# Kernel tuning notes

Measured on AMD Instinct MI355X. Metric: run time of the kernel, lower is better.

The kernel has to match this reference:

```python
import jax, jax.numpy as jnp
import numpy as np

N_NODES = 50000
N_EDGES = 800000
F_IN = 32
H = 128
N_REL = 4
MAX_DEG = 10
N_GRAPHS = 64
N_BLOCKS = 2


def setup_inputs() -> dict:
    key = jax.random.key(0)
    ks = jax.random.split(key, 20)
    s = 0.05
    return {
        "x": jax.random.normal(ks[0], (N_NODES, F_IN), jnp.float32),
        "edge_index": jax.random.randint(ks[1], (2, N_EDGES), 0, N_NODES, dtype=jnp.int32),
        "edge_attr": jax.random.randint(ks[2], (N_EDGES,), 0, N_REL, dtype=jnp.int32),
        "batch_idx": jnp.sort(jax.random.randint(ks[3], (N_NODES,), 0, N_GRAPHS, dtype=jnp.int32)),
        "embed_W": jax.random.normal(ks[4], (F_IN, H), jnp.float32) * s,
        "embed_b": jax.random.normal(ks[5], (H,), jnp.float32) * s,
        "rgcn_Wrel": jax.random.normal(ks[6], (N_BLOCKS, N_REL, H, H), jnp.float32) * s,
        "rgcn_Wroot": jax.random.normal(ks[7], (N_BLOCKS, H, H), jnp.float32) * s,
        "rgcn_b": jax.random.normal(ks[8], (N_BLOCKS, H), jnp.float32) * s,
        "mf_Wl": jax.random.normal(ks[9], (N_BLOCKS, MAX_DEG + 1, H, H), jnp.float32) * s,
        "mf_bl": jax.random.normal(ks[10], (N_BLOCKS, MAX_DEG + 1, H), jnp.float32) * s,
        "mf_Wr": jax.random.normal(ks[11], (N_BLOCKS, MAX_DEG + 1, H, H), jnp.float32) * s,
        "lin1_W": jax.random.normal(ks[12], (H, H), jnp.float32) * s,
        "lin1_b": jax.random.normal(ks[13], (H,), jnp.float32) * s,
        "lin2_W": jax.random.normal(ks[14], (H, 1), jnp.float32) * s,
        "lin2_b": jax.random.normal(ks[15], (1,), jnp.float32) * s,
    }


def _rgcn(x, src, dst, rel, Wrel, Wroot, b):
    # PyG RGCNConv with default aggr='mean': per-relation mean over incoming
    # edges, then per-relation weight, plus root transform and bias.
    seg = dst * N_REL + rel  # composite segment id: (node, relation)
    agg = jax.ops.segment_sum(x[src], seg, num_segments=N_NODES * N_REL)
    cnt = jax.ops.segment_sum(jnp.ones((seg.shape[0],), x.dtype), seg,
                              num_segments=N_NODES * N_REL)
    agg = (agg / jnp.maximum(cnt, 1.0)[:, None]).reshape(N_NODES, N_REL, H)
    return jnp.einsum('nrh,rho->no', agg, Wrel) + x @ Wroot + b


def _mfconv(x, src, dst, Wl, bl, Wr):
    # PyG MFConv: sum-aggregate neighbors, then per-degree-bucket linear heads
    # (degree = in-degree clamped to MAX_DEG); lin_r applied to root x (no bias).
    h = jax.ops.segment_sum(x[src], dst, num_segments=N_NODES)  # [N,H]
    deg = jax.ops.segment_sum(jnp.ones((src.shape[0],), jnp.int32), dst,
                              num_segments=N_NODES)
    deg = jnp.minimum(deg, MAX_DEG)  # [N]
    # out_all: [D+1, N, H] candidate outputs, one per degree bucket
    out_all = (jnp.einsum('nh,dho->dno', h, Wl)
               + jnp.einsum('nh,dho->dno', x, Wr)
               + bl[:, None, :])
    return jnp.take_along_axis(out_all, deg[None, :, None], axis=0)[0]


def reference(x, edge_index, edge_attr, batch_idx, embed_W, embed_b,
              rgcn_Wrel, rgcn_Wroot, rgcn_b, mf_Wl, mf_bl, mf_Wr,
              lin1_W, lin1_b, lin2_W, lin2_b):
    src, dst = edge_index[0], edge_index[1]
    h = x @ embed_W + embed_b
    for blk in range(N_BLOCKS):
        if blk > 0:  # first block uses Identity instead of ReLU
            h = jax.nn.relu(h)
        h = _rgcn(h, src, dst, edge_attr, rgcn_Wrel[blk], rgcn_Wroot[blk], rgcn_b[blk])
        h = jax.nn.relu(h)
        h = _mfconv(h, src, dst, mf_Wl[blk], mf_bl[blk], mf_Wr[blk])
    g = jax.ops.segment_sum(h, batch_idx, num_segments=N_GRAPHS)  # global_add_pool
    g = jax.nn.relu(g @ lin1_W + lin1_b)
    return g @ lin2_W + lin2_b
```

## Files before the change

### kernel.cpp

```cpp
#include <hip/hip_runtime.h>
#include <hip/hip_bf16.h>

#define NRELS 4
#define MAXDEG 10
#define NBUCK 11
#define POOL_CHUNKS 8

typedef __attribute__((ext_vector_type(8))) short s16x8;
typedef __attribute__((ext_vector_type(4))) float f32x4;
typedef __attribute__((ext_vector_type(8))) unsigned short u16x8;

__device__ inline unsigned short f2b(float f) {
  __hip_bfloat16 h = __float2bfloat16(f);
  return *reinterpret_cast<unsigned short*>(&h);
}
__device__ inline float b2f(unsigned short u) {
  union { unsigned int i; float f; } v;
  v.i = ((unsigned int)u) << 16;
  return v.f;
}
__device__ inline float blo(unsigned int v) {
  union { unsigned int i; float f; } x;
  x.i = v << 16;
  return x.f;
}
__device__ inline float bhi(unsigned int v) {
  union { unsigned int i; float f; } x;
  x.i = v & 0xffff0000u;
  return x.f;
}

typedef __attribute__((address_space(3))) unsigned int lds_uint;
typedef __attribute__((address_space(1))) const unsigned int glob_uint;
__device__ __forceinline__ void gld_lds16(const void* g, void* l) {
  __builtin_amdgcn_global_load_lds((glob_uint*)g, (lds_uint*)l, 16, 0, 0);
}

__global__ __launch_bounds__(512) void coarse_count(const int* __restrict__ dst,
                                                    int* __restrict__ bhist, int E) {
  __shared__ int lh[512];
  int t = threadIdx.x;
  lh[t] = 0;
  __syncthreads();
  int base = blockIdx.x * 4096;
  int lim = E - base;
  if (lim > 4096) lim = 4096;
  for (int i = t; i < lim; i += 512) atomicAdd(&lh[dst[base + i] >> 7], 1);
  __syncthreads();
  if (lh[t]) atomicAdd(&bhist[t], lh[t]);
}

__global__ __launch_bounds__(512) void coarse_scan(const int* __restrict__ bhist,
                                                   int* __restrict__ boff,
                                                   int* __restrict__ bcur, int NB, int E) {
  __shared__ int sd[512];
  int t = threadIdx.x;
  int v = (t < NB) ? bhist[t] : 0;
  sd[t] = v;
  __syncthreads();
  for (int o = 1; o < 512; o <<= 1) {
    int x = (t >= o) ? sd[t - o] : 0;
    __syncthreads();
    sd[t] += x;
    __syncthreads();
  }
  if (t < NB) {
    int st = sd[t] - v;
    boff[t] = st;
    bcur[t] = st;
  }
  if (t == 0) boff[NB] = E;
}

__global__ __launch_bounds__(512) void coarse_scatter(
    const int* __restrict__ src, const int* __restrict__ dst, const int* __restrict__ rel,
    int* __restrict__ bcur, uint2* __restrict__ ebuf, int E) {
  __shared__ int lhist[512];
  __shared__ int lstart[512];
  __shared__ int lcur[512];
  __shared__ int gbase[512];
  __shared__ uint2 stage[4096];
  int t = threadIdx.x;
  lhist[t] = 0;
  __syncthreads();
  int base = blockIdx.x * 4096;
  int lim = E - base;
  if (lim > 4096) lim = 4096;
  for (int i = t; i < lim; i += 512) atomicAdd(&lhist[dst[base + i] >> 7], 1);
  __syncthreads();
  int myc = lhist[t];
  lstart[t] = myc;
  __syncthreads();
  for (int o = 1; o < 512; o <<= 1) {
    int x = (t >= o) ? lstart[t - o] : 0;
    __syncthreads();
    lstart[t] += x;
    __syncthreads();
  }
  int incl = lstart[t];
  __syncthreads();
  lstart[t] = incl - myc;
  lcur[t] = 0;
  if (myc > 0) gbase[t] = atomicAdd(&bcur[t], myc);
  __syncthreads();
  for (int i = t; i < lim; i += 512) {
    int e = base + i;
    int d = dst[e];
    int b = d >> 7;
    int slot = lstart[b] + atomicAdd(&lcur[b], 1);
    stage[slot] = make_uint2((unsigned)(d * 4 + rel[e]), (unsigned)src[e]);
  }
  __syncthreads();
  for (int i = t; i < lim; i += 512) {
    uint2 val = stage[i];
    int b = (int)(val.x >> 9);
    ebuf[gbase[b] + (i - lstart[b])] = val;
  }
}

__global__ __launch_bounds__(512) void fine_count_scan(
    const uint2* __restrict__ ebuf, const int* __restrict__ boff, int* __restrict__ cnt,
    int* __restrict__ seg_start, float* __restrict__ inv, int* __restrict__ deg,
    int* __restrict__ bucket, int* __restrict__ hist, int NSEG) {
  __shared__ int lh[512];
  __shared__ int sc[512];
  __shared__ int lbh[16];
  int t = threadIdx.x;
  int b = blockIdx.x;
  lh[t] = 0;
  if (t < 16) lbh[t] = 0;
  __syncthreads();
  int s = boff[b], e = boff[b + 1];
  for (int i = s + t; i < e; i += 512) atomicAdd(&lh[ebuf[i].x & 511], 1);
  __syncthreads();
  int v = lh[t];
  sc[t] = v;
  __syncthreads();
  for (int o = 1; o < 512; o <<= 1) {
    int x = (t >= o) ? sc[t - o] : 0;
    __syncthreads();
    sc[t] += x;
    __syncthreads();
  }
  int gseg = b * 512 + t;
  if (gseg < NSEG) {
    cnt[gseg] = v;
    seg_start[gseg] = s + sc[t] - v;
    inv[gseg] = 1.0f / (float)(v > 1 ? v : 1);
    if ((t & 3) == 0) {
      int d = sc[t + 3] - sc[t] + v;
      int n = gseg >> 2;
      deg[n] = d;
      int bk = d < MAXDEG ? d : MAXDEG;
      bucket[n] = bk;
      atomicAdd(&lbh[bk], 1);
    }
  }
  __syncthreads();
  if (t < NBUCK && lbh[t]) atomicAdd(&hist[t], lbh[t]);
}

__global__ __launch_bounds__(512) void place_local(const uint2* __restrict__ ebuf,
                                                   const int* __restrict__ boff,
                                                   const int* __restrict__ seg_start,
                                                   int* __restrict__ csr, int NSEG) {
  __shared__ int lcur[512];
  int t = threadIdx.x;
  int b = blockIdx.x;
  int gseg = b * 512 + t;
  lcur[t] = (gseg < NSEG) ? seg_start[gseg] : 0;
  __syncthreads();
  int s = boff[b], e = boff[b + 1];
  for (int i = s + t; i < e; i += 512) {
    uint2 v = ebuf[i];
    int pos = atomicAdd(&lcur[v.x & 511], 1);
    csr[pos] = (int)v.y;
  }
}

__global__ void build_perm(const int* __restrict__ bucket, const int* __restrict__ hist,
                           int* __restrict__ fill, int* __restrict__ perm, int N) {
  __shared__ int soff[NBUCK];
  if (threadIdx.x == 0) {
    int acc = 0;
    for (int b = 0; b < NBUCK; b++) {
      soff[b] = acc;
      acc += ((hist[b] + 63) >> 6) << 6;
    }
  }
  __syncthreads();
  int n = blockIdx.x * 256 + threadIdx.x;
  int b = (n < N) ? bucket[n] : -1;
  int lane = threadIdx.x & 63;
  for (int bb = 0; bb < NBUCK; bb++) {
    unsigned long long m = __ballot(b == bb);
    if (m == 0ULL) continue;
    int leader = __ffsll(m) - 1;
    int base = 0;
    if (lane == leader) base = atomicAdd(&fill[bb], __popcll(m));
    base = __shfl(base, leader);
    if (b == bb) {
      int idx = __popcll(m & ((1ULL << lane) - 1ULL));
      perm[soff[bb] + base + idx] = n;
    }
  }
}

__global__ void conv_weights(const float* __restrict__ Wrel, const float* __restrict__ Wroot,
                             const float* __restrict__ Wl, const float* __restrict__ Wr,
                             const float* __restrict__ embW, unsigned short* __restrict__ Bt,
                             unsigned short* __restrict__ Btm, unsigned short* __restrict__ Bte) {
  const int R1 = 2 * 128 * 640;
  const int R2 = R1 + 2 * 11 * 128 * 256;
  const int R3 = R2 + 128 * 32;
  int t = blockIdx.x * 256 + threadIdx.x;
  if (t < R1) {
    int blk = t / 81920;
    int rem = t % 81920;
    int n = rem / 640;
    int k = rem % 640;
    float v;
    if (k < 512)
      v = Wrel[(size_t)blk * 65536 + (size_t)k * 128 + n];
    else
      v = Wroot[(size_t)blk * 16384 + (size_t)(k - 512) * 128 + n];
    Bt[t] = f2b(v);
    return;
  }
  if (t < R2) {
    int t2 = t - R1;
    int k = t2 & 255;
    int n = (t2 >> 8) & 127;
    int bb = (t2 >> 15) % 11;
    int blk = t2 / (11 * 128 * 256);
    float v;
    if (k < 128)
      v = Wl[(((size_t)blk * 11 + bb) * 128 + k) * 128 + n];
    else
      v = Wr[(((size_t)blk * 11 + bb) * 128 + (k - 128)) * 128 + n];
    Btm[t2] = f2b(v);
    return;
  }
  if (t < R3) {
    int t3 = t - R2;
    int n = t3 >> 5, k = t3 & 31;
    Bte[t3] = f2b(embW[(size_t)k * 128 + n]);
  }
}

#define ACC8(v)                                   \
  do {                                            \
    a0 += blo((v).x); a1 += bhi((v).x);           \
    a2 += blo((v).y); a3 += bhi((v).y);           \
    a4 += blo((v).z); a5 += bhi((v).z);           \
    a6 += blo((v).w); a7 += bhi((v).w);           \
  } while (0)

__global__ __launch_bounds__(256) void rgcn_gather(
    const unsigned short* __restrict__ hb, const int* __restrict__ csr,
    const int* __restrict__ seg_start, const int* __restrict__ cnt,
    const float* __restrict__ inv, const int* __restrict__ perm,
    unsigned short* __restrict__ ahat, int total) {
  int half = blockIdx.x & 1;
  int i = (blockIdx.x >> 1) * 32 + (threadIdx.x >> 3);
  if (i >= total) return;
  int n = perm[i];
  if (n < 0) return;
  int c8 = half * 64 + (threadIdx.x & 7) * 8;
#pragma unroll
  for (int r = 0; r < 4; r++) {
    int seg = n * 4 + r;
    int st = seg_start[seg], cn = cnt[seg];
    float w = inv[seg];
    float a0 = 0.f, a1 = 0.f, a2 = 0.f, a3 = 0.f, a4 = 0.f, a5 = 0.f, a6 = 0.f, a7 = 0.f;
    int ii = 0;
    for (; ii + 4 <= cn; ii += 4) {
      int p0 = csr[st + ii], p1 = csr[st + ii + 1];
      int p2 = csr[st + ii + 2], p3 = csr[st + ii + 3];
      uint4 v0 = *(const uint4*)(hb + (size_t)p0 * 128 + c8);
      uint4 v1 = *(const uint4*)(hb + (size_t)p1 * 128 + c8);
      uint4 v2 = *(const uint4*)(hb + (size_t)p2 * 128 + c8);
      uint4 v3 = *(const uint4*)(hb + (size_t)p3 * 128 + c8);
      ACC8(v0);
      ACC8(v1);
      ACC8(v2);
      ACC8(v3);
    }
    if (ii + 2 <= cn) {
      int p0 = csr[st + ii], p1 = csr[st + ii + 1];
      uint4 v0 = *(const uint4*)(hb + (size_t)p0 * 128 + c8);
      uint4 v1 = *(const uint4*)(hb + (size_t)p1 * 128 + c8);
      ACC8(v0);
      ACC8(v1);
      ii += 2;
    }
    if (ii < cn) {
      uint4 v0 = *(const uint4*)(hb + (size_t)csr[st + ii] * 128 + c8);
      ACC8(v0);
    }
    uint4 o;
    o.x = (unsigned int)f2b(a0 * w) | ((unsigned int)f2b(a1 * w) << 16);
    o.y = (unsigned int)f2b(a2 * w) | ((unsigned int)f2b(a3 * w) << 16);
    o.z = (unsigned int)f2b(a4 * w) | ((unsigned int)f2b(a5 * w) << 16);
    o.w = (unsigned int)f2b(a6 * w) | ((unsigned int)f2b(a7 * w) << 16);
    *(uint4*)(ahat + (size_t)i * 512 + r * 128 + c8) = o;
  }
}

__global__ __launch_bounds__(256) void mf_gather(
    const unsigned short* __restrict__ hb, const int* __restrict__ csr,
    const int* __restrict__ seg_start, const int* __restrict__ deg,
    const int* __restrict__ perm, unsigned short* __restrict__ amf, int total) {
  int half = blockIdx.x & 1;
  int i = (blockIdx.x >> 1) * 32 + (threadIdx.x >> 3);
  if (i >= total) return;
  int n = perm[i];
  if (n < 0) return;
  int c8 = half * 64 + (threadIdx.x & 7) * 8;
  int st = seg_start[n * 4], dg = deg[n];
  float a0 = 0.f, a1 = 0.f, a2 = 0.f, a3 = 0.f, a4 = 0.f, a5 = 0.f, a6 = 0.f, a7 = 0.f;
  int i2 = 0;
  for (; i2 + 4 <= dg; i2 += 4) {
    int p0 = csr[st + i2], p1 = csr[st + i2 + 1];
    int p2 = csr[st + i2 + 2], p3 = csr[st + i2 + 3];
    uint4 v0 = *(const uint4*)(hb + (size_t)p0 * 128 + c8);
    uint4 v1 = *(const uint4*)(hb + (size_t)p1 * 128 + c8);
    uint4 v2 = *(const uint4*)(hb + (size_t)p2 * 128 + c8);
    uint4 v3 = *(const uint4*)(hb + (size_t)p3 * 128 + c8);
    ACC8(v0);
    ACC8(v1);
    ACC8(v2);
    ACC8(v3);
  }
  if (i2 + 2 <= dg) {
    int p0 = csr[st + i2], p1 = csr[st + i2 + 1];
    uint4 v0 = *(const uint4*)(hb + (size_t)p0 * 128 + c8);
    uint4 v1 = *(const uint4*)(hb + (size_t)p1 * 128 + c8);
    ACC8(v0);
    ACC8(v1);
    i2 += 2;
  }
  if (i2 < dg) {
    uint4 v0 = *(const uint4*)(hb + (size_t)csr[st + i2] * 128 + c8);
    ACC8(v0);
  }
  uint4 o;
  o.x = (unsigned int)f2b(a0) | ((unsigned int)f2b(a1) << 16);
  o.y = (unsigned int)f2b(a2) | ((unsigned int)f2b(a3) << 16);
  o.z = (unsigned int)f2b(a4) | ((unsigned int)f2b(a5) << 16);
  o.w = (unsigned int)f2b(a6) | ((unsigned int)f2b(a7) << 16);
  *(uint4*)(amf + (size_t)i * 128 + c8) = o;
}

__global__ __launch_bounds__(256) void rgcn_mfma(const unsigned short* __restrict__ A,
                                                 const unsigned short* __restrict__ hroot,
                                                 const unsigned short* __restrict__ Bt,
                                                 const float* __restrict__ bias,
                                                 const int* __restrict__ perm,
                                                 unsigned short* __restrict__ out) {
  __shared__ unsigned char As[8192];
  __shared__ unsigned char Bs[16384];
  __shared__ int nodes[64];
  int t = threadIdx.x;
  int m0 = blockIdx.x * 64;
  if (t >= 64 && t < 128) nodes[t - 64] = perm[m0 + t - 64];
  __syncthreads();
  int lane = t & 63, wave = t >> 6;
  int row = lane & 15, quad = lane >> 4;
  int nh = wave * 32;
  f32x4 acc[2][4];
#pragma unroll
  for (int i = 0; i < 2; i++)
#pragma unroll
    for (int j = 0; j < 4; j++) acc[i][j] = (f32x4){0.f, 0.f, 0.f, 0.f};

  for (int kt = 0; kt < 10; kt++) {
    int kb2 = kt * 128;
#pragma unroll
    for (int s = 0; s < 2; s++) {
      int o = s * 4096 + t * 16;
      int r = o >> 7, c = ((o >> 4) & 7) ^ (r & 7);
      const char* gsrc;
      if (kt < 8) {
        gsrc = (const char*)A + (size_t)(m0 + r) * 1024 + kb2 + c * 16;
      } else {
        int nd = nodes[r];
        if (nd < 0) nd = 0;
        gsrc = (const char*)hroot + (size_t)nd * 256 + (kb2 - 1024) + c * 16;
      }
      gld_lds16(gsrc, As + o);
    }
#pragma unroll
    for (int s = 0; s < 4; s++) {
      int o = s * 4096 + t * 16;
      int r = o >> 7, c = ((o >> 4) & 7) ^ (r & 7);
      gld_lds16((const char*)Bt + (size_t)r * 1280 + kb2 + c * 16, Bs + o);
    }
    __syncthreads();
#pragma unroll
    for (int ks = 0; ks < 2; ks++) {
      int cch = ks * 4 + quad;
      s16x8 af[4], bf[2];
#pragma unroll
      for (int mt = 0; mt < 4; mt++) {
        int R = mt * 16 + row;
        af[mt] = *(const s16x8*)(As + R * 128 + ((cch ^ (R & 7)) << 4));
      }
#pragma unroll
      for (int nt = 0; nt < 2; nt++) {
        int R = nh + nt * 16 + row;
        bf[nt] = *(const s16x8*)(Bs + R * 128 + ((cch ^ (R & 7)) << 4));
      }
#pragma unroll
      for (int nt = 0; nt < 2; nt++)
#pragma unroll
        for (int mt = 0; mt < 4; mt++)
          acc[nt][mt] = __builtin_amdgcn_mfma_f32_16x16x32_bf16(af[mt], bf[nt], acc[nt][mt], 0, 0, 0);
    }
    __syncthreads();
  }
#pragma unroll
  for (int nt = 0; nt < 2; nt++) {
    int n = nh + nt * 16 + row;
    float bv = bias[n];
#pragma unroll
    for (int mt = 0; mt < 4; mt++) {
#pragma unroll
      for (int r4 = 0; r4 < 4; r4++) {
        int nd = nodes[mt * 16 + quad * 4 + r4];
        if (nd >= 0) out[(size_t)nd * 128 + n] = f2b(fmaxf(acc[nt][mt][r4] + bv, 0.f));
      }
    }
  }
}

__global__ __launch_bounds__(256) void mf_mfma(const unsigned short* __restrict__ A,
                                               const unsigned short* __restrict__ hroot,
                                               const unsigned short* __restrict__ Bt,
                                               const float* __restrict__ bl,
                                               const int* __restrict__ perm,
                                               const int* __restrict__ hist,
                                               unsigned short* __restrict__ out, int relu_out) {
  __shared__ unsigned char As[8192];
  __shared__ unsigned char Bs[16384];
  __shared__ int soff[NBUCK + 1];
  __shared__ int nodes[64];
  int t = threadIdx.x;
  int m0 = blockIdx.x * 64;
  if (t == 0) {
    int acc = 0;
    for (int b2 = 0; b2 < NBUCK; b2++) {
      soff[b2] = acc;
      acc += ((hist[b2] + 63) >> 6) << 6;
    }
    soff[NBUCK] = acc;
  }
  if (t >= 64 && t < 128) nodes[t - 64] = perm[m0 + t - 64];
  __syncthreads();
  if (m0 >= soff[NBUCK]) return;
  int b = 0;
  while (b < 10 && m0 >= soff[b + 1]) b++;
  const unsigned short* Bb = Bt + (size_t)b * 128 * 256;
  const float* bb = bl + b * 128;
  int lane = t & 63, wave = t >> 6;
  int row = lane & 15, quad = lane >> 4;
  int nh = wave * 32;
  f32x4 acc[2][4];
#pragma unroll
  for (int i = 0; i < 2; i++)
#pragma unroll
    for (int j = 0; j < 4; j++) acc[i][j] = (f32x4){0.f, 0.f, 0.f, 0.f};

  for (int kt = 0; kt < 4; kt++) {
    int kb2 = kt * 128;
#pragma unroll
    for (int s = 0; s < 2; s++) {
      int o = s * 4096 + t * 16;
      int r = o >> 7, c = ((o >> 4) & 7) ^ (r & 7);
      const char* gsrc;
      if (kt < 2) {
        gsrc = (const char*)A + (size_t)(m0 + r) * 256 + kb2 + c * 16;
      } else {
        int nd = nodes[r];
        if (nd < 0) nd = 0;
        gsrc = (const char*)hroot + (size_t)nd * 256 + (kb2 - 512) + c * 16;
      }
      gld_lds16(gsrc, As + o);
    }
#pragma unroll
    for (int s = 0; s < 4; s++) {
      int o = s * 4096 + t * 16;
      int r = o >> 7, c = ((o >> 4) & 7) ^ (r & 7);
      gld_lds16((const char*)Bb + (size_t)r * 512 + kb2 + c * 16, Bs + o);
    }
    __syncthreads();
#pragma unroll
    for (int ks = 0; ks < 2; ks++) {
      int cch = ks * 4 + quad;
      s16x8 af[4], bf[2];
#pragma unroll
      for (int mt = 0; mt < 4; mt++) {
        int R = mt * 16 + row;
        af[mt] = *(const s16x8*)(As + R * 128 + ((cch ^ (R & 7)) << 4));
      }
#pragma unroll
      for (int nt = 0; nt < 2; nt++) {
        int R = nh + nt * 16 + row;
        bf[nt] = *(const s16x8*)(Bs + R * 128 + ((cch ^ (R & 7)) << 4));
      }
#pragma unroll
      for (int nt = 0; nt < 2; nt++)
#pragma unroll
        for (int mt = 0; mt < 4; mt++)
          acc[nt][mt] = __builtin_amdgcn_mfma_f32_16x16x32_bf16(af[mt], bf[nt], acc[nt][mt], 0, 0, 0);
    }
    __syncthreads();
  }
#pragma unroll
  for (int nt = 0; nt < 2; nt++) {
    int n = nh + nt * 16 + row;
    float bv = bb[n];
#pragma unroll
    for (int mt = 0; mt < 4; mt++) {
#pragma unroll
      for (int r4 = 0; r4 < 4; r4++) {
        int nd = nodes[mt * 16 + quad * 4 + r4];
        if (nd >= 0) {
          float v = acc[nt][mt][r4] + bv;
          if (relu_out) v = fmaxf(v, 0.f);
          out[(size_t)nd * 128 + n] = f2b(v);
        }
      }
    }
  }
}

__global__ __launch_bounds__(256) void embed_mfma(const float* __restrict__ x,
                                                  const unsigned short* __restrict__ Bte,
                                                  const float* __restrict__ bias,
                                                  unsigned short* __restrict__ out, int N) {
  __shared__ unsigned char As[64 * 80];
  __shared__ unsigned char Bs[128 * 80];
  int t = threadIdx.x;
  int m0 = blockIdx.x * 64;
  {
    int r = t >> 2, s = t & 3;
    int gr = m0 + r;
    if (gr >= N) gr = N - 1;
    const float* xp = x + (size_t)gr * 32 + s * 8;
    float4 f0 = *(const float4*)xp;
    float4 f1 = *(const float4*)(xp + 4);
    u16x8 o;
    o[0] = f2b(f0.x); o[1] = f2b(f0.y); o[2] = f2b(f0.z); o[3] = f2b(f0.w);
    o[4] = f2b(f1.x); o[5] = f2b(f1.y); o[6] = f2b(f1.z); o[7] = f2b(f1.w);
    *(u16x8*)(As + r * 80 + s * 16) = o;
  }
  {
    int n = t >> 1, s = t & 1;
    const unsigned short* bp = Bte + (size_t)n * 32 + s * 16;
    uint4 v0 = *(const uint4*)bp;
    uint4 v1 = *(const uint4*)(bp + 8);
    *(uint4*)(Bs + n * 80 + s * 32) = v0;
    *(uint4*)(Bs + n * 80 + s * 32 + 16) = v1;
  }
  __syncthreads();
  int lane = t & 63, wave = t >> 6;
  int row = lane & 15, quad = lane >> 4;
  int nh = wave * 32;
  f32x4 acc[2][4];
#pragma unroll
  for (int i = 0; i < 2; i++)
#pragma unroll
    for (int j = 0; j < 4; j++) acc[i][j] = (f32x4){0.f, 0.f, 0.f, 0.f};
  s16x8 af[4], bf[2];
#pragma unroll
  for (int mt = 0; mt < 4; mt++) {
    int R = mt * 16 + row;
    af[mt] = *(const s16x8*)(As + R * 80 + quad * 16);
  }
#pragma unroll
  for (int nt = 0; nt < 2; nt++) {
    int R = nh + nt * 16 + row;
    bf[nt] = *(const s16x8*)(Bs + R * 80 + quad * 16);
  }
#pragma unroll
  for (int nt = 0; nt < 2; nt++)
#pragma unroll
    for (int mt = 0; mt < 4; mt++)
      acc[nt][mt] = __builtin_amdgcn_mfma_f32_16x16x32_bf16(af[mt], bf[nt], acc[nt][mt], 0, 0, 0);
#pragma unroll
  for (int nt = 0; nt < 2; nt++) {
    int n = nh + nt * 16 + row;
    float bv = bias[n];
#pragma unroll
    for (int mt = 0; mt < 4; mt++) {
#pragma unroll
      for (int r4 = 0; r4 < 4; r4++) {
        int m = m0 + mt * 16 + quad * 4 + r4;
        if (m < N) out[(size_t)m * 128 + n] = f2b(acc[nt][mt][r4] + bv);
      }
    }
  }
}

__global__ void pool2(const unsigned short* __restrict__ h, const int* __restrict__ batch,
                      float* __restrict__ g, int N, int G) {
  int gr = blockIdx.x / POOL_CHUNKS;
  int ck = blockIdx.x % POOL_CHUNKS;
  int c = threadIdx.x;
  int lo = 0, hi = N;
  while (lo < hi) {
    int m = (lo + hi) >> 1;
    if (batch[m] < gr) lo = m + 1; else hi = m;
  }
  int s = lo;
  lo = s; hi = N;
  while (lo < hi) {
    int m = (lo + hi) >> 1;
    if (batch[m] < gr + 1) lo = m + 1; else hi = m;
  }
  int e = lo;
  int len = e - s;
  int a = s + (int)(((long long)len * ck) / POOL_CHUNKS);
  int b = s + (int)(((long long)len * (ck + 1)) / POOL_CHUNKS);
  float sum = 0.f;
  for (int n = a; n < b; n++) sum += b2f(h[(size_t)n * 128 + c]);
  if (b > a) atomicAdd(&g[gr * 128 + c], sum);
}

__global__ void head_kernel(const float* __restrict__ g, const float* __restrict__ W1,
                            const float* __restrict__ b1, const float* __restrict__ W2,
                            const float* __restrict__ b2, float* __restrict__ out) {
  int bg = blockIdx.x;
  int o = threadIdx.x;
  __shared__ float gs[128];
  __shared__ float red[128];
  gs[o] = g[bg * 128 + o];
  __syncthreads();
  float acc = b1[o];
  for (int k = 0; k < 128; k++) acc += gs[k] * W1[k * 128 + o];
  acc = fmaxf(acc, 0.f);
  red[o] = acc * W2[o];
  __syncthreads();
  for (int s = 64; s > 0; s >>= 1) {
    if (o < s) red[o] += red[o + s];
    __syncthreads();
  }
  if (o == 0) out[bg] = red[0] + b2[0];
}

extern "C" void kernel_launch(void* const* d_in, const int* in_sizes, int n_in,
                              void* d_out, int out_size, void* d_ws, size_t ws_size,
                              hipStream_t stream) {
  const float* x = (const float*)d_in[0];
  const int* ei = (const int*)d_in[1];
  const int* ea = (const int*)d_in[2];
  const int* batch = (const int*)d_in[3];
  const float* embW = (const float*)d_in[4];
  const float* embB = (const float*)d_in[5];
  const float* Wrel = (const float*)d_in[6];
  const float* Wroot = (const float*)d_in[7];
  const float* rb = (const float*)d_in[8];
  const float* Wl = (const float*)d_in[9];
  const float* bl = (const float*)d_in[10];
  const float* Wr = (const float*)d_in[11];
  const float* l1W = (const float*)d_in[12];
  const float* l1b = (const float*)d_in[13];
  const float* l2W = (const float*)d_in[14];
  const float* l2b = (const float*)d_in[15];
  float* out = (float*)d_out;

  int N = in_sizes[0] / 32;
  int E = in_sizes[2];
  int G = out_size;
  int NSEG = N * 4;
  int NB = (N + 127) >> 7;

  char* p = (char*)d_ws;
  auto alloc = [&](size_t bytes) {
    char* r = p;
    p += (bytes + 255) & ~(size_t)255;
    return r;
  };
  int permCap = ((N + 63) / 64 + NBUCK) * 64;
  unsigned short* h_bf = (unsigned short*)alloc((size_t)N * 128 * 2);
  unsigned short* h2_bf = (unsigned short*)alloc((size_t)N * 128 * 2);
  unsigned short* ahat = (unsigned short*)alloc((size_t)permCap * 512 * 2);
  unsigned short* amf = (unsigned short*)alloc((size_t)permCap * 128 * 2);
  unsigned short* Btr = (unsigned short*)alloc((size_t)2 * 128 * 640 * 2);
  unsigned short* Btm = (unsigned short*)alloc((size_t)2 * 11 * 128 * 256 * 2);
  unsigned short* Bte = (unsigned short*)alloc((size_t)128 * 32 * 2);
  float* inv = (float*)alloc((size_t)NSEG * 4);
  int* cnt = (int*)alloc((size_t)NSEG * 4);
  int* seg_start = (int*)alloc((size_t)NSEG * 4);
  int* csr = (int*)alloc((size_t)E * 4);
  uint2* ebuf = (uint2*)alloc((size_t)E * 8);
  int* deg = (int*)alloc((size_t)N * 4);
  int* bucket = (int*)alloc((size_t)N * 4);
  int* perm = (int*)alloc((size_t)permCap * 4);
  int* boff = (int*)alloc(516 * 4);
  int* bcur = (int*)alloc(512 * 4);
  size_t zeroBytes = 8192 + (size_t)G * 128 * 4;
  char* zb = alloc(zeroBytes);
  int* bhist = (int*)zb;
  int* hist = (int*)(zb + 4096);
  int* fill = (int*)(zb + 4224);
  float* g = (float*)(zb + 8192);

  hipMemsetAsync(zb, 0, zeroBytes, stream);
  hipMemsetAsync(perm, 0xFF, (size_t)permCap * 4, stream);

  const int* src = ei;
  const int* dst = ei + E;

  int sblocks = (E + 4095) / 4096;
  coarse_count<<<sblocks, 512, 0, stream>>>(dst, bhist, E);
  coarse_scan<<<1, 512, 0, stream>>>(bhist, boff, bcur, NB, E);
  coarse_scatter<<<sblocks, 512, 0, stream>>>(src, dst, ea, bcur, ebuf, E);
  fine_count_scan<<<NB, 512, 0, stream>>>(ebuf, boff, cnt, seg_start, inv, deg, bucket, hist,
                                          NSEG);
  build_perm<<<(N + 255) / 256, 256, 0, stream>>>(bucket, hist, fill, perm, N);
  place_local<<<NB, 512, 0, stream>>>(ebuf, boff, seg_start, csr, NSEG);
  int convTotal = 2 * 128 * 640 + 2 * 11 * 128 * 256 + 128 * 32;
  conv_weights<<<(convTotal + 255) / 256, 256, 0, stream>>>(Wrel, Wroot, Wl, Wr, embW, Btr,
                                                            Btm, Bte);

  embed_mfma<<<(N + 63) / 64, 256, 0, stream>>>(x, Bte, embB, h_bf, N);

  int mfblocks = permCap / 64;
  int gblocks = ((permCap + 31) / 32) * 2;
  for (int blk = 0; blk < 2; blk++) {
    rgcn_gather<<<gblocks, 256, 0, stream>>>(h_bf, csr, seg_start, cnt, inv, perm, ahat,
                                             permCap);
    rgcn_mfma<<<mfblocks, 256, 0, stream>>>(ahat, h_bf, Btr + (size_t)blk * 81920,
                                            rb + blk * 128, perm, h2_bf);
    mf_gather<<<gblocks, 256, 0, stream>>>(h2_bf, csr, seg_start, deg, perm, amf, permCap);
    mf_mfma<<<mfblocks, 256, 0, stream>>>(amf, h2_bf, Btm + (size_t)blk * 11 * 128 * 256,
                                          bl + (size_t)blk * 11 * 128, perm, hist, h_bf,
                                          (blk == 0) ? 1 : 0);
  }
  pool2<<<G * POOL_CHUNKS, 128, 0, stream>>>(h_bf, batch, g, N, G);
  head_kernel<<<G, 128, 0, stream>>>(g, l1W, l1b, l2W, l2b, out);
}
```

Baseline: 406.2 us.

## Fuse CSR build kernels, widen MFMA row tiles, vectorize gather and pool loads

Merges the coarse count and scan into one kernel using a last-block-done counter, and folds CSR placement into the fine count/scan kernel, removing two launches. Doubles the row tile of the RGCN and MFConv MFMA kernels from 64 to 128 nodes per block, with degree buckets padded to 128. This halves the number of B-weight reloads per node but gives fewer blocks and more padding. It also loads per-node segment metadata as int4/float4 in the gather, and makes pooling read two bf16 values per thread with two row groups.

Result: slower. 415.8 us (+2.4%).

```diff
diff --git a/kernel.cpp b/kernel.cpp
--- a/kernel.cpp
+++ b/kernel.cpp
@@ -36,9 +36,11 @@
   __builtin_amdgcn_global_load_lds((glob_uint*)g, (lds_uint*)l, 16, 0, 0);
 }
 
-__global__ __launch_bounds__(512) void coarse_count(const int* __restrict__ dst,
-                                                    int* __restrict__ bhist, int E) {
+__global__ __launch_bounds__(512) void coarse_count_scan(
+    const int* __restrict__ dst, int* __restrict__ bhist, int* __restrict__ boff,
+    int* __restrict__ bcur, int* __restrict__ done, int NB, int E, int nblocks) {
   __shared__ int lh[512];
+  __shared__ int lastf;
   int t = threadIdx.x;
   lh[t] = 0;
   __syncthreads();
@@ -48,24 +50,22 @@
   for (int i = t; i < lim; i += 512) atomicAdd(&lh[dst[base + i] >> 7], 1);
   __syncthreads();
   if (lh[t]) atomicAdd(&bhist[t], lh[t]);
-}
-
-__global__ __launch_bounds__(512) void coarse_scan(const int* __restrict__ bhist,
-                                                   int* __restrict__ boff,
-                                                   int* __restrict__ bcur, int NB, int E) {
-  __shared__ int sd[512];
-  int t = threadIdx.x;
-  int v = (t < NB) ? bhist[t] : 0;
-  sd[t] = v;
+  __threadfence();
+  __syncthreads();
+  if (t == 0) lastf = (atomicAdd(done, 1) == nblocks - 1) ? 1 : 0;
+  __syncthreads();
+  if (!lastf) return;
+  int v = (t < NB) ? atomicAdd(&bhist[t], 0) : 0;
+  lh[t] = v;
   __syncthreads();
   for (int o = 1; o < 512; o <<= 1) {
-    int x = (t >= o) ? sd[t - o] : 0;
-    __syncthreads();
-    sd[t] += x;
+    int x = (t >= o) ? lh[t - o] : 0;
+    __syncthreads();
+    lh[t] += x;
     __syncthreads();
   }
   if (t < NB) {
-    int st = sd[t] - v;
+    int st = lh[t] - v;
     boff[t] = st;
     bcur[t] = st;
   }
@@ -118,12 +118,13 @@
   }
 }
 
-__global__ __launch_bounds__(512) void fine_count_scan(
+__global__ __launch_bounds__(512) void fine_place(
     const uint2* __restrict__ ebuf, const int* __restrict__ boff, int* __restrict__ cnt,
     int* __restrict__ seg_start, float* __restrict__ inv, int* __restrict__ deg,
-    int* __restrict__ bucket, int* __restrict__ hist, int NSEG) {
+    int* __restrict__ bucket, int* __restrict__ hist, int* __restrict__ csr, int NSEG) {
   __shared__ int lh[512];
   __shared__ int sc[512];
+  __shared__ int lcur[512];
   __shared__ int lbh[16];
   int t = threadIdx.x;
   int b = blockIdx.x;
@@ -143,9 +144,11 @@
     __syncthreads();
   }
   int gseg = b * 512 + t;
+  int mystart = s + sc[t] - v;
+  lcur[t] = mystart;
   if (gseg < NSEG) {
     cnt[gseg] = v;
-    seg_start[gseg] = s + sc[t] - v;
+    seg_start[gseg] = mystart;
     inv[gseg] = 1.0f / (float)(v > 1 ? v : 1);
     if ((t & 3) == 0) {
       int d = sc[t + 3] - sc[t] + v;
@@ -158,23 +161,10 @@
   }
   __syncthreads();
   if (t < NBUCK && lbh[t]) atomicAdd(&hist[t], lbh[t]);
-}
-
-__global__ __launch_bounds__(512) void place_local(const uint2* __restrict__ ebuf,
-                                                   const int* __restrict__ boff,
-                                                   const int* __restrict__ seg_start,
-                                                   int* __restrict__ csr, int NSEG) {
-  __shared__ int lcur[512];
-  int t = threadIdx.x;
-  int b = blockIdx.x;
-  int gseg = b * 512 + t;
-  lcur[t] = (gseg < NSEG) ? seg_start[gseg] : 0;
-  __syncthreads();
-  int s = boff[b], e = boff[b + 1];
   for (int i = s + t; i < e; i += 512) {
-    uint2 v = ebuf[i];
-    int pos = atomicAdd(&lcur[v.x & 511], 1);
-    csr[pos] = (int)v.y;
+    uint2 vv = ebuf[i];
+    int pos = atomicAdd(&lcur[vv.x & 511], 1);
+    csr[pos] = (int)vv.y;
   }
 }
 
@@ -185,7 +175,7 @@
     int acc = 0;
     for (int b = 0; b < NBUCK; b++) {
       soff[b] = acc;
-      acc += ((hist[b] + 63) >> 6) << 6;
+      acc += ((hist[b] + 127) >> 7) << 7;
     }
   }
   __syncthreads();
@@ -267,11 +257,16 @@
   int n = perm[i];
   if (n < 0) return;
   int c8 = half * 64 + (threadIdx.x & 7) * 8;
+  int4 st4 = *(const int4*)(seg_start + (size_t)n * 4);
+  int4 cn4 = *(const int4*)(cnt + (size_t)n * 4);
+  float4 w4 = *(const float4*)(inv + (size_t)n * 4);
+  int sts[4] = {st4.x, st4.y, st4.z, st4.w};
+  int cns[4] = {cn4.x, cn4.y, cn4.z, cn4.w};
+  float ws[4] = {w4.x, w4.y, w4.z, w4.w};
 #pragma unroll
   for (int r = 0; r < 4; r++) {
-    int seg = n * 4 + r;
-    int st = seg_start[seg], cn = cnt[seg];
-    float w = inv[seg];
+    int st = sts[r], cn = cns[r];
+    float w = ws[r];
     float a0 = 0.f, a1 = 0.f, a2 = 0.f, a3 = 0.f, a4 = 0.f, a5 = 0.f, a6 = 0.f, a7 = 0.f;
     int ii = 0;
     for (; ii + 4 <= cn; ii += 4) {
@@ -358,26 +353,26 @@
                                                  const float* __restrict__ bias,
                                                  const int* __restrict__ perm,
                                                  unsigned short* __restrict__ out) {
-  __shared__ unsigned char As[8192];
+  __shared__ unsigned char As[16384];
   __shared__ unsigned char Bs[16384];
-  __shared__ int nodes[64];
+  __shared__ int nodes[128];
   int t = threadIdx.x;
-  int m0 = blockIdx.x * 64;
-  if (t >= 64 && t < 128) nodes[t - 64] = perm[m0 + t - 64];
+  int m0 = blockIdx.x * 128;
+  if (t < 128) nodes[t] = perm[m0 + t];
   __syncthreads();
   int lane = t & 63, wave = t >> 6;
   int row = lane & 15, quad = lane >> 4;
   int nh = wave * 32;
-  f32x4 acc[2][4];
+  f32x4 acc[2][8];
 #pragma unroll
   for (int i = 0; i < 2; i++)
 #pragma unroll
-    for (int j = 0; j < 4; j++) acc[i][j] = (f32x4){0.f, 0.f, 0.f, 0.f};
+    for (int j = 0; j < 8; j++) acc[i][j] = (f32x4){0.f, 0.f, 0.f, 0.f};
 
   for (int kt = 0; kt < 10; kt++) {
     int kb2 = kt * 128;
 #pragma unroll
-    for (int s = 0; s < 2; s++) {
+    for (int s = 0; s < 4; s++) {
       int o = s * 4096 + t * 16;
       int r = o >> 7, c = ((o >> 4) & 7) ^ (r & 7);
       const char* gsrc;
@@ -400,9 +395,9 @@
 #pragma unroll
     for (int ks = 0; ks < 2; ks++) {
       int cch = ks * 4 + quad;
-      s16x8 af[4], bf[2];
-#pragma unroll
-      for (int mt = 0; mt < 4; mt++) {
+      s16x8 af[8], bf[2];
+#pragma unroll
+      for (int mt = 0; mt < 8; mt++) {
         int R = mt * 16 + row;
         af[mt] = *(const s16x8*)(As + R * 128 + ((cch ^ (R & 7)) << 4));
       }
@@ -414,7 +409,7 @@
 #pragma unroll
       for (int nt = 0; nt < 2; nt++)
 #pragma unroll
-        for (int mt = 0; mt < 4; mt++)
+        for (int mt = 0; mt < 8; mt++)
           acc[nt][mt] = __builtin_amdgcn_mfma_f32_16x16x32_bf16(af[mt], bf[nt], acc[nt][mt], 0, 0, 0);
     }
     __syncthreads();
@@ -424,7 +419,7 @@
     int n = nh + nt * 16 + row;
     float bv = bias[n];
 #pragma unroll
-    for (int mt = 0; mt < 4; mt++) {
+    for (int mt = 0; mt < 8; mt++) {
 #pragma unroll
       for (int r4 = 0; r4 < 4; r4++) {
         int nd = nodes[mt * 16 + quad * 4 + r4];
@@ -441,21 +436,21 @@
                                                const int* __restrict__ perm,
                                                const int* __restrict__ hist,
                                                unsigned short* __restrict__ out, int relu_out) {
-  __shared__ unsigned char As[8192];
+  __shared__ unsigned char As[16384];
   __shared__ unsigned char Bs[16384];
   __shared__ int soff[NBUCK + 1];
-  __shared__ int nodes[64];
+  __shared__ int nodes[128];
   int t = threadIdx.x;
-  int m0 = blockIdx.x * 64;
+  int m0 = blockIdx.x * 128;
   if (t == 0) {
     int acc = 0;
     for (int b2 = 0; b2 < NBUCK; b2++) {
       soff[b2] = acc;
-      acc += ((hist[b2] + 63) >> 6) << 6;
+      acc += ((hist[b2] + 127) >> 7) << 7;
     }
     soff[NBUCK] = acc;
   }
-  if (t >= 64 && t < 128) nodes[t - 64] = perm[m0 + t - 64];
+  if (t < 128) nodes[t] = perm[m0 + t];
   __syncthreads();
   if (m0 >= soff[NBUCK]) return;
   int b = 0;
@@ -465,16 +460,16 @@
   int lane = t & 63, wave = t >> 6;
   int row = lane & 15, quad = lane >> 4;
   int nh = wave * 32;
-  f32x4 acc[2][4];
+  f32x4 acc[2][8];
 #pragma unroll
   for (int i = 0; i < 2; i++)
 #pragma unroll
-    for (int j = 0; j < 4; j++) acc[i][j] = (f32x4){0.f, 0.f, 0.f, 0.f};
+    for (int j = 0; j < 8; j++) acc[i][j] = (f32x4){0.f, 0.f, 0.f, 0.f};
 
   for (int kt = 0; kt < 4; kt++) {
     int kb2 = kt * 128;
 #pragma unroll
-    for (int s = 0; s < 2; s++) {
+    for (int s = 0; s < 4; s++) {
       int o = s * 4096 + t * 16;
       int r = o >> 7, c = ((o >> 4) & 7) ^ (r & 7);
       const char* gsrc;
@@ -497,9 +492,9 @@
 #pragma unroll
     for (int ks = 0; ks < 2; ks++) {
       int cch = ks * 4 + quad;
-      s16x8 af[4], bf[2];
-#pragma unroll
-      for (int mt = 0; mt < 4; mt++) {
+      s16x8 af[8], bf[2];
+#pragma unroll
+      for (int mt = 0; mt < 8; mt++) {
         int R = mt * 16 + row;
         af[mt] = *(const s16x8*)(As + R * 128 + ((cch ^ (R & 7)) << 4));
       }
@@ -511,7 +506,7 @@
 #pragma unroll
       for (int nt = 0; nt < 2; nt++)
 #pragma unroll
-        for (int mt = 0; mt < 4; mt++)
+        for (int mt = 0; mt < 8; mt++)
           acc[nt][mt] = __builtin_amdgcn_mfma_f32_16x16x32_bf16(af[mt], bf[nt], acc[nt][mt], 0, 0, 0);
     }
     __syncthreads();
@@ -521,7 +516,7 @@
     int n = nh + nt * 16 + row;
     float bv = bb[n];
 #pragma unroll
-    for (int mt = 0; mt < 4; mt++) {
+    for (int mt = 0; mt < 8; mt++) {
 #pragma unroll
       for (int r4 = 0; r4 < 4; r4++) {
         int nd = nodes[mt * 16 + quad * 4 + r4];
@@ -607,7 +602,8 @@
                       float* __restrict__ g, int N, int G) {
   int gr = blockIdx.x / POOL_CHUNKS;
   int ck = blockIdx.x % POOL_CHUNKS;
-  int c = threadIdx.x;
+  int t = threadIdx.x;
+  int lane = t & 63, grp = t >> 6;
   int lo = 0, hi = N;
   while (lo < hi) {
     int m = (lo + hi) >> 1;
@@ -623,9 +619,16 @@
   int len = e - s;
   int a = s + (int)(((long long)len * ck) / POOL_CHUNKS);
   int b = s + (int)(((long long)len * (ck + 1)) / POOL_CHUNKS);
-  float sum = 0.f;
-  for (int n = a; n < b; n++) sum += b2f(h[(size_t)n * 128 + c]);
-  if (b > a) atomicAdd(&g[gr * 128 + c], sum);
+  float s0 = 0.f, s1 = 0.f;
+  for (int n = a + grp; n < b; n += 2) {
+    unsigned int v = *(const unsigned int*)(h + (size_t)n * 128 + lane * 2);
+    s0 += blo(v);
+    s1 += bhi(v);
+  }
+  if (b > a + grp) {
+    atomicAdd(&g[gr * 128 + lane * 2], s0);
+    atomicAdd(&g[gr * 128 + lane * 2 + 1], s1);
+  }
 }
 
 __global__ void head_kernel(const float* __restrict__ g, const float* __restrict__ W1,
@@ -682,7 +685,7 @@
     p += (bytes + 255) & ~(size_t)255;
     return r;
   };
-  int permCap = ((N + 63) / 64 + NBUCK) * 64;
+  int permCap = ((N + 127) / 128 + NBUCK) * 128;
   unsigned short* h_bf = (unsigned short*)alloc((size_t)N * 128 * 2);
   unsigned short* h2_bf = (unsigned short*)alloc((size_t)N * 128 * 2);
   unsigned short* ahat = (unsigned short*)alloc((size_t)permCap * 512 * 2);
@@ -705,6 +708,7 @@
   int* bhist = (int*)zb;
   int* hist = (int*)(zb + 4096);
   int* fill = (int*)(zb + 4224);
+  int* done = (int*)(zb + 4352);
   float* g = (float*)(zb + 8192);
 
   hipMemsetAsync(zb, 0, zeroBytes, stream);
@@ -714,20 +718,18 @@
   const int* dst = ei + E;
 
   int sblocks = (E + 4095) / 4096;
-  coarse_count<<<sblocks, 512, 0, stream>>>(dst, bhist, E);
-  coarse_scan<<<1, 512, 0, stream>>>(bhist, boff, bcur, NB, E);
+  coarse_count_scan<<<sblocks, 512, 0, stream>>>(dst, bhist, boff, bcur, done, NB, E, sblocks);
   coarse_scatter<<<sblocks, 512, 0, stream>>>(src, dst, ea, bcur, ebuf, E);
-  fine_count_scan<<<NB, 512, 0, stream>>>(ebuf, boff, cnt, seg_start, inv, deg, bucket, hist,
-                                          NSEG);
+  fine_place<<<NB, 512, 0, stream>>>(ebuf, boff, cnt, seg_start, inv, deg, bucket, hist, csr,
+                                     NSEG);
   build_perm<<<(N + 255) / 256, 256, 0, stream>>>(bucket, hist, fill, perm, N);
-  place_local<<<NB, 512, 0, stream>>>(ebuf, boff, seg_start, csr, NSEG);
   int convTotal = 2 * 128 * 640 + 2 * 11 * 128 * 256 + 128 * 32;
   conv_weights<<<(convTotal + 255) / 256, 256, 0, stream>>>(Wrel, Wroot, Wl, Wr, embW, Btr,
                                                             Btm, Bte);
 
   embed_mfma<<<(N + 63) / 64, 256, 0, stream>>>(x, Bte, embB, h_bf, N);
 
-  int mfblocks = permCap / 64;
+  int mfblocks = permCap / 128;
   int gblocks = ((permCap + 31) / 32) * 2;
   for (int blk = 0; blk < 2; blk++) {
     rgcn_gather<<<gblocks, 256, 0, stream>>>(h_bf, csr, seg_start, cnt, inv, perm, ahat,
```
